# Optimization experiments

Measured on AMD Instinct MI355X. Metric: run time of the kernel, lower is better.

The kernel has to match this reference:

```python
import jax, jax.numpy as jnp
import numpy as np

E, T, IN, OUT = 8, 16384, 1024, 1024  # n_groups, total_tokens, in_features, out_features


def setup_inputs() -> dict:
    key = jax.random.key(0)
    kx, kw, ks = jax.random.split(key, 3)
    x = jax.random.normal(kx, (T, IN), dtype=jnp.float32)
    # kaiming_uniform-ish scale for weight [E, OUT, IN]
    weight = jax.random.normal(kw, (E, OUT, IN), dtype=jnp.float32) * (1.0 / np.sqrt(IN))
    # ragged segment lengths that sum exactly to T (random cut points)
    cuts = jnp.sort(jax.random.randint(ks, (E - 1,), 0, T + 1)).astype(jnp.int32)
    seg_lens = jnp.diff(
        jnp.concatenate([jnp.zeros((1,), jnp.int32), cuts, jnp.full((1,), T, jnp.int32)])
    )
    return {"x": x, "weight": weight, "seg_lens": seg_lens}


def reference(x, weight, seg_lens):
    # Grouped GEMM: row t of x is multiplied by weight[g(t)].T where g(t) is the
    # segment (expert) that token t falls into per seg_lens. trans_b=True.
    n_groups = weight.shape[0]
    bounds = jnp.cumsum(seg_lens)                                  # [E]
    seg_id = jnp.searchsorted(bounds, jnp.arange(x.shape[0]), side="right")  # [T]
    y = jnp.zeros((x.shape[0], weight.shape[1]), dtype=x.dtype)
    for e in range(n_groups):  # small fixed loop over groups
        y = y + jnp.where((seg_id == e)[:, None], x @ weight[e].T, 0)
    return y
```

## Files before the change

kernel.cpp:

```cpp
#include <hip/hip_runtime.h>

#define T_TOK  16384
#define IN_F   1024
#define OUT_F  1024
#define NE     8

typedef __bf16 bf16;
typedef bf16  bf16x4 __attribute__((ext_vector_type(4)));
typedef bf16  bf16x8 __attribute__((ext_vector_type(8)));
typedef float f32x4  __attribute__((ext_vector_type(4)));

#define BM 256
#define BN 256
#define BK 64
#define GTHREADS 512
#define NBLOCKS 256
#define KCH (IN_F / BK)
#define SP_BLOCKS 112

#define CVT_THREADS 256
#define NX_CHUNKS (T_TOK * IN_F / 4)
#define NW_CHUNKS (NE * OUT_F * IN_F / 4)
#define NCVT_CHUNKS (NX_CHUNKS + NW_CHUNKS)

__global__ __launch_bounds__(CVT_THREADS)
void cvt_and_zero(const float* __restrict__ x, const float* __restrict__ w,
                  bf16* __restrict__ xb, bf16* __restrict__ wb,
                  const int* __restrict__ seg_lens, float* __restrict__ out)
{
    int r64 = T_TOK;
    {
        int slots = 0, start = 0;
        #pragma unroll
        for (int e = 0; e < NE; ++e) {
            int len = seg_lens[e];
            int nt  = (len + BM - 1) >> 8;
            if (slots <= 64 && slots + nt > 64) {
                r64 = start + (64 - slots) * BM;
            }
            slots += nt;
            start += len;
        }
    }
    const int zero_chunks = (T_TOK - r64) * (OUT_F / 4);
    const int zbase       = r64 * (OUT_F / 4);
    const int tot         = NCVT_CHUNKS + zero_chunks;

    for (int i = blockIdx.x * CVT_THREADS + threadIdx.x; i < tot;
         i += gridDim.x * CVT_THREADS) {
        if (i < NCVT_CHUNKS) {
            const bool isx = (i < NX_CHUNKS);
            const int  j   = isx ? i : i - NX_CHUNKS;
            f32x4 v = isx ? ((const f32x4*)x)[j] : ((const f32x4*)w)[j];
            bf16x4 h;
            #pragma unroll
            for (int k = 0; k < 4; ++k) h[k] = (bf16)v[k];
            if (isx) ((bf16x4*)xb)[j] = h;
            else     ((bf16x4*)wb)[j] = h;
        } else {
            f32x4 z = {0.f, 0.f, 0.f, 0.f};
            ((f32x4*)out)[zbase + (i - NCVT_CHUNKS)] = z;
        }
    }
}

__device__ __forceinline__ void gld_lds16(const bf16* g, bf16* l) {
    __builtin_amdgcn_global_load_lds(
        (const __attribute__((address_space(1))) void*)g,
        (__attribute__((address_space(3))) void*)l,
        16, 0, 0);
}

__device__ __forceinline__ void resolve_slot(const int* sl, int slot,
                                             int& e_sel, int& row0, int& rows)
{
    e_sel = -1; row0 = 0; rows = 0;
    int start = 0, acct = 0;
    #pragma unroll
    for (int e = 0; e < NE; ++e) {
        int len = sl[e];
        int nt  = (len + BM - 1) >> 8;
        if (e_sel < 0 && slot >= acct && slot < acct + nt) {
            e_sel = e;
            row0  = start + (slot - acct) * BM;
            int rm = start + len - row0;
            rows = rm < BM ? rm : BM;
        }
        acct  += nt;
        start += len;
    }
}

__global__ __launch_bounds__(GTHREADS)
void grouped_gemm_main(const bf16* __restrict__ xb,
                       const bf16* __restrict__ wb,
                       const int*  __restrict__ seg_lens,
                       float* __restrict__ out)
{
    __shared__ __align__(16) bf16 As[2][BM * BK];
    __shared__ __align__(16) bf16 Bs[2][BN * BK];

    const int tile = blockIdx.x;
    const int slot = tile >> 2;
    const int col0 = (tile & 3) << 8;

    int sl[NE];
    #pragma unroll
    for (int e = 0; e < NE; ++e) sl[e] = seg_lens[e];

    int e_sel, row0, rows;
    resolve_slot(sl, slot, e_sel, row0, rows);
    if (e_sel < 0) return;

    const int tid  = threadIdx.x;
    const int lane = tid & 63;
    const int wave = tid >> 6;
    const int wr   = wave >> 2;
    const int wc   = wave & 3;
    const int quad = lane >> 4;
    const int l16  = lane & 15;
    const int rq   = lane >> 3;
    const int ke   = (lane & 7) * 8;
    const int q0   = wave * 4;

    const bf16* wbase = wb + ((size_t)e_sel * OUT_F + (size_t)col0) * IN_F;

    const bf16* ga[4];
    const bf16* gb[4];
    #pragma unroll
    for (int i = 0; i < 4; ++i) {
        int q  = wave * 4 + i;
        int ra = row0 + q * 8 + rq;
        if (ra > T_TOK - 1) ra = T_TOK - 1;
        ga[i] = xb + (size_t)ra * IN_F + ke;
        gb[i] = wbase + (size_t)(q * 8 + rq) * IN_F + ke;
    }

    f32x4 acc[8][4] = {};

    #pragma unroll
    for (int i = 0; i < 4; ++i) {
        gld_lds16(ga[i], &As[0][(q0 + i) * 512]);
        gld_lds16(gb[i], &Bs[0][(q0 + i) * 512]);
    }
    __syncthreads();

    int cur = 0;
    for (int ks = 0; ks < KCH; ++ks) {
        const int kn = (ks + 1) * BK;
        if (kn < IN_F) {
            #pragma unroll
            for (int i = 0; i < 4; ++i) {
                gld_lds16(ga[i] + kn, &As[cur ^ 1][(q0 + i) * 512]);
                gld_lds16(gb[i] + kn, &Bs[cur ^ 1][(q0 + i) * 512]);
            }
        }

        #pragma unroll
        for (int kk = 0; kk < 2; ++kk) {
            bf16x8 af[8], bfr[4];
            #pragma unroll
            for (int t = 0; t < 8; ++t)
                af[t] = *(const bf16x8*)(
                    &As[cur][(wr * 128 + t * 16 + l16) * BK + kk * 32 + quad * 8]);
            #pragma unroll
            for (int v = 0; v < 4; ++v)
                bfr[v] = *(const bf16x8*)(
                    &Bs[cur][(wc * 64 + v * 16 + l16) * BK + kk * 32 + quad * 8]);
            #pragma unroll
            for (int t = 0; t < 8; ++t)
                #pragma unroll
                for (int v = 0; v < 4; ++v)
                    acc[t][v] = __builtin_amdgcn_mfma_f32_16x16x32_bf16(
                        af[t], bfr[v], acc[t][v], 0, 0, 0);
        }

        __syncthreads();
        cur ^= 1;
    }

    #pragma unroll
    for (int t = 0; t < 8; ++t) {
        #pragma unroll
        for (int r = 0; r < 4; ++r) {
            int row = wr * 128 + t * 16 + quad * 4 + r;
            if (row < rows) {
                size_t ob = (size_t)(row0 + row) * OUT_F + col0 + wc * 64;
                #pragma unroll
                for (int v = 0; v < 4; ++v)
                    out[ob + v * 16 + l16] = acc[t][v][r];
            }
        }
    }
}

__global__ __launch_bounds__(GTHREADS)
void grouped_gemm_surplus(const bf16* __restrict__ xb,
                          const bf16* __restrict__ wb,
                          const int*  __restrict__ seg_lens,
                          float* __restrict__ out)
{
    __shared__ __align__(16) bf16 As[2][BM * BK];
    __shared__ __align__(16) bf16 Bs[2][BN * BK];

    const int tile   = NBLOCKS + (blockIdx.x >> 2);
    const int kslice = blockIdx.x & 3;

    int sl[NE];
    #pragma unroll
    for (int e = 0; e < NE; ++e) sl[e] = seg_lens[e];

    int n_slots = 0;
    #pragma unroll
    for (int e = 0; e < NE; ++e) n_slots += (sl[e] + BM - 1) >> 8;
    const int L = n_slots * (OUT_F / BN);
    if (tile >= L) return;

    const int slot = tile >> 2;
    const int col0 = (tile & 3) << 8;
    int e_sel, row0, rows;
    resolve_slot(sl, slot, e_sel, row0, rows);

    const int tid  = threadIdx.x;
    const int lane = tid & 63;
    const int wave = tid >> 6;
    const int wr   = wave >> 2;
    const int wc   = wave & 3;
    const int quad = lane >> 4;
    const int l16  = lane & 15;
    const int rq   = lane >> 3;
    const int ke   = (lane & 7) * 8;
    const int q0   = wave * 4;

    const bf16* wbase = wb + ((size_t)e_sel * OUT_F + (size_t)col0) * IN_F;

    const bf16* ga[4];
    const bf16* gb[4];
    #pragma unroll
    for (int i = 0; i < 4; ++i) {
        int q  = wave * 4 + i;
        int ra = row0 + q * 8 + rq;
        if (ra > T_TOK - 1) ra = T_TOK - 1;
        ga[i] = xb + (size_t)ra * IN_F + ke;
        gb[i] = wbase + (size_t)(q * 8 + rq) * IN_F + ke;
    }

    f32x4 acc[8][4] = {};

    const int kb0 = kslice * 4 * BK;

    #pragma unroll
    for (int i = 0; i < 4; ++i) {
        gld_lds16(ga[i] + kb0, &As[0][(q0 + i) * 512]);
        gld_lds16(gb[i] + kb0, &Bs[0][(q0 + i) * 512]);
    }
    __syncthreads();

    #pragma unroll
    for (int j = 0; j < 4; ++j) {
        const int cur = j & 1;
        if (j < 3) {
            const int kn = kb0 + (j + 1) * BK;
            #pragma unroll
            for (int i = 0; i < 4; ++i) {
                gld_lds16(ga[i] + kn, &As[cur ^ 1][(q0 + i) * 512]);
                gld_lds16(gb[i] + kn, &Bs[cur ^ 1][(q0 + i) * 512]);
            }
        }

        #pragma unroll
        for (int kk = 0; kk < 2; ++kk) {
            bf16x8 af[8], bfr[4];
            #pragma unroll
            for (int t = 0; t < 8; ++t)
                af[t] = *(const bf16x8*)(
                    &As[cur][(wr * 128 + t * 16 + l16) * BK + kk * 32 + quad * 8]);
            #pragma unroll
            for (int v = 0; v < 4; ++v)
                bfr[v] = *(const bf16x8*)(
                    &Bs[cur][(wc * 64 + v * 16 + l16) * BK + kk * 32 + quad * 8]);
            #pragma unroll
            for (int t = 0; t < 8; ++t)
                #pragma unroll
                for (int v = 0; v < 4; ++v)
                    acc[t][v] = __builtin_amdgcn_mfma_f32_16x16x32_bf16(
                        af[t], bfr[v], acc[t][v], 0, 0, 0);
        }

        __syncthreads();
    }

    #pragma unroll
    for (int t = 0; t < 8; ++t) {
        #pragma unroll
        for (int r = 0; r < 4; ++r) {
            int row = wr * 128 + t * 16 + quad * 4 + r;
            if (row < rows) {
                size_t ob = (size_t)(row0 + row) * OUT_F + col0 + wc * 64;
                #pragma unroll
                for (int v = 0; v < 4; ++v)
                    unsafeAtomicAdd(&out[ob + v * 16 + l16], acc[t][v][r]);
            }
        }
    }
}

#define FBM 128
#define FBK 32
#define FTHREADS 256
#define FROW_SLOTS 136

__global__ __launch_bounds__(FTHREADS)
void grouped_gemm_f32io_bf16(const float* __restrict__ x,
                             const float* __restrict__ wgt,
                             const int*  __restrict__ seg_lens,
                             float* __restrict__ out)
{
    __shared__ __align__(16) bf16 Asf[FBM * FBK];
    __shared__ __align__(16) bf16 Bsf[FBM * FBK];

    const int m    = blockIdx.y;
    const int col0 = blockIdx.x * FBM;

    int e_sel = -1, row0 = 0, rows = 0;
    {
        int start = 0, acct = 0;
        #pragma unroll
        for (int e = 0; e < NE; ++e) {
            int len = seg_lens[e];
            int nt  = (len + FBM - 1) >> 7;
            if (e_sel < 0 && m >= acct && m < acct + nt) {
                e_sel = e;
                row0  = start + (m - acct) * FBM;
                int rem = start + len - row0;
                rows = rem < FBM ? rem : FBM;
            }
            acct  += nt;
            start += len;
        }
    }
    if (e_sel < 0) return;

    const int tid  = threadIdx.x;
    const int lane = tid & 63;
    const int wave = tid >> 6;
    const int wm   = (wave >> 1) * 64;
    const int wn   = (wave & 1) * 64;
    const int quad = lane >> 4;
    const int l16  = lane & 15;

    const float* wbase = wgt + ((size_t)e_sel * OUT_F + (size_t)col0) * IN_F;

    f32x4 acc[4][4] = {};

    for (int k0 = 0; k0 < IN_F; k0 += FBK) {
        f32x4 a_st[4], b_st[4];
        #pragma unroll
        for (int t = 0; t < 4; ++t) {
            int c  = t * FTHREADS + tid;
            int rg = row0 + (c >> 3);
            if (rg > T_TOK - 1) rg = T_TOK - 1;
            a_st[t] = *(const f32x4*)(x + (size_t)rg * IN_F + k0 + (c & 7) * 4);
            b_st[t] = *(const f32x4*)(wbase + (size_t)(c >> 3) * IN_F + k0 + (c & 7) * 4);
        }

        __syncthreads();

        #pragma unroll
        for (int t = 0; t < 4; ++t) {
            int c = t * FTHREADS + tid;
            bf16x4 ha, hb;
            #pragma unroll
            for (int j = 0; j < 4; ++j) { ha[j] = (bf16)a_st[t][j]; hb[j] = (bf16)b_st[t][j]; }
            *(bf16x4*)(&Asf[(c >> 3) * FBK + (c & 7) * 4]) = ha;
            *(bf16x4*)(&Bsf[(c >> 3) * FBK + (c & 7) * 4]) = hb;
        }
        __syncthreads();

        bf16x8 af[4], bfr[4];
        #pragma unroll
        for (int t = 0; t < 4; ++t)
            af[t] = *(const bf16x8*)(&Asf[(wm + t * 16 + l16) * FBK + quad * 8]);
        #pragma unroll
        for (int v = 0; v < 4; ++v)
            bfr[v] = *(const bf16x8*)(&Bsf[(wn + v * 16 + l16) * FBK + quad * 8]);

        #pragma unroll
        for (int t = 0; t < 4; ++t)
            #pragma unroll
            for (int v = 0; v < 4; ++v)
                acc[t][v] = __builtin_amdgcn_mfma_f32_16x16x32_bf16(
                    af[t], bfr[v], acc[t][v], 0, 0, 0);
    }

    #pragma unroll
    for (int t = 0; t < 4; ++t) {
        #pragma unroll
        for (int r = 0; r < 4; ++r) {
            int row = wm + t * 16 + quad * 4 + r;
            if (row < rows) {
                size_t ob = (size_t)(row0 + row) * OUT_F + col0;
                #pragma unroll
                for (int v = 0; v < 4; ++v)
                    out[ob + wn + v * 16 + l16] = acc[t][v][r];
            }
        }
    }
}

extern "C" void kernel_launch(void* const* d_in, const int* in_sizes, int n_in,
                              void* d_out, int out_size, void* d_ws, size_t ws_size,
                              hipStream_t stream) {
    const float* x   = (const float*)d_in[0];
    const float* wgt = (const float*)d_in[1];
    const int*   seg = (const int*)d_in[2];
    float* out = (float*)d_out;

    const size_t xbytes = (size_t)T_TOK * IN_F * sizeof(bf16);
    const size_t wbytes = (size_t)NE * OUT_F * IN_F * sizeof(bf16);

    if (ws_size >= xbytes + wbytes) {
        bf16* xb = (bf16*)d_ws;
        bf16* wb = (bf16*)((char*)d_ws + xbytes);
        cvt_and_zero<<<dim3(2048, 1, 1), dim3(CVT_THREADS, 1, 1), 0, stream>>>(
            x, wgt, xb, wb, seg, out);
        grouped_gemm_main<<<dim3(NBLOCKS, 1, 1), dim3(GTHREADS, 1, 1), 0, stream>>>(
            xb, wb, seg, out);
        grouped_gemm_surplus<<<dim3(SP_BLOCKS, 1, 1), dim3(GTHREADS, 1, 1), 0, stream>>>(
            xb, wb, seg, out);
    } else {
        grouped_gemm_f32io_bf16<<<dim3(OUT_F / FBM, FROW_SLOTS, 1),
                                  dim3(FTHREADS, 1, 1), 0, stream>>>(x, wgt, seg, out);
    }
}
```

Baseline: 215.0 us.

## Swizzle LDS tiles, use explicit vmcnt waits in GEMM pipeline, widen conversion vectors

The main GEMM kernel now XOR-swizzles the k-chunk position of each row when loading into LDS and applies the matching swizzle on fragment reads, to remove LDS bank conflicts. The k-loop is restructured so the next tile's loads are issued first, then a partial s_waitcnt vmcnt(8) and raw barriers with sched_barrier fences gate the compute, letting the prefetch stay in flight during MFMA work. The conversion kernel processes 8 elements per thread instead of 4. The hand-written waitcnt and barriers depend on exact load counts and ordering, so any mismatch could give incorrect results.

```diff
diff --git a/kernel.cpp b/kernel.cpp
--- a/kernel.cpp
+++ b/kernel.cpp
@@ -19,9 +19,9 @@
 #define SP_BLOCKS 112
 
 #define CVT_THREADS 256
-#define NX_CHUNKS (T_TOK * IN_F / 4)
-#define NW_CHUNKS (NE * OUT_F * IN_F / 4)
-#define NCVT_CHUNKS (NX_CHUNKS + NW_CHUNKS)
+#define NX8 (T_TOK * IN_F / 8)
+#define NW8 (NE * OUT_F * IN_F / 8)
+#define NCVT8 (NX8 + NW8)
 
 __global__ __launch_bounds__(CVT_THREADS)
 void cvt_and_zero(const float* __restrict__ x, const float* __restrict__ w,
@@ -42,24 +42,27 @@
             start += len;
         }
     }
-    const int zero_chunks = (T_TOK - r64) * (OUT_F / 4);
-    const int zbase       = r64 * (OUT_F / 4);
-    const int tot         = NCVT_CHUNKS + zero_chunks;
+    const int zero8 = (T_TOK - r64) * (OUT_F / 8);
+    const int zb8   = r64 * (OUT_F / 8);
+    const int tot   = NCVT8 + zero8;
 
     for (int i = blockIdx.x * CVT_THREADS + threadIdx.x; i < tot;
          i += gridDim.x * CVT_THREADS) {
-        if (i < NCVT_CHUNKS) {
-            const bool isx = (i < NX_CHUNKS);
-            const int  j   = isx ? i : i - NX_CHUNKS;
-            f32x4 v = isx ? ((const f32x4*)x)[j] : ((const f32x4*)w)[j];
-            bf16x4 h;
-            #pragma unroll
-            for (int k = 0; k < 4; ++k) h[k] = (bf16)v[k];
-            if (isx) ((bf16x4*)xb)[j] = h;
-            else     ((bf16x4*)wb)[j] = h;
+        if (i < NCVT8) {
+            const bool isx = (i < NX8);
+            const int  j   = isx ? i : i - NX8;
+            f32x4 v0 = isx ? ((const f32x4*)x)[2*j]   : ((const f32x4*)w)[2*j];
+            f32x4 v1 = isx ? ((const f32x4*)x)[2*j+1] : ((const f32x4*)w)[2*j+1];
+            bf16x8 h;
+            #pragma unroll
+            for (int k = 0; k < 4; ++k) { h[k] = (bf16)v0[k]; h[4+k] = (bf16)v1[k]; }
+            if (isx) ((bf16x8*)xb)[j] = h;
+            else     ((bf16x8*)wb)[j] = h;
         } else {
             f32x4 z = {0.f, 0.f, 0.f, 0.f};
-            ((f32x4*)out)[zbase + (i - NCVT_CHUNKS)] = z;
+            const int j = zb8 + (i - NCVT8);
+            ((f32x4*)out)[2*j]   = z;
+            ((f32x4*)out)[2*j+1] = z;
         }
     }
 }
@@ -91,6 +94,31 @@
     }
 }
 
+__device__ __forceinline__ void mfma_step(const bf16* __restrict__ Ab,
+                                          const bf16* __restrict__ Bb,
+                                          f32x4 (&acc)[8][4],
+                                          int wr, int wc, int l16, int quad,
+                                          int swz8)
+{
+    #pragma unroll
+    for (int kk = 0; kk < 2; ++kk) {
+        const int ce = (kk * 32 + quad * 8) ^ swz8;
+        bf16x8 af[8], bfr[4];
+        #pragma unroll
+        for (int t = 0; t < 8; ++t)
+            af[t] = *(const bf16x8*)(Ab + (wr * 128 + t * 16 + l16) * BK + ce);
+        #pragma unroll
+        for (int v = 0; v < 4; ++v)
+            bfr[v] = *(const bf16x8*)(Bb + (wc * 64 + v * 16 + l16) * BK + ce);
+        #pragma unroll
+        for (int t = 0; t < 8; ++t)
+            #pragma unroll
+            for (int v = 0; v < 4; ++v)
+                acc[t][v] = __builtin_amdgcn_mfma_f32_16x16x32_bf16(
+                    af[t], bfr[v], acc[t][v], 0, 0, 0);
+    }
+}
+
 __global__ __launch_bounds__(GTHREADS)
 void grouped_gemm_main(const bf16* __restrict__ xb,
                        const bf16* __restrict__ wb,
@@ -120,8 +148,10 @@
     const int quad = lane >> 4;
     const int l16  = lane & 15;
     const int rq   = lane >> 3;
-    const int ke   = (lane & 7) * 8;
     const int q0   = wave * 4;
+    const int swz8 = (l16 & 7) * 8;
+
+    const int ke_s = (((lane & 7) ^ rq) * 8);
 
     const bf16* wbase = wb + ((size_t)e_sel * OUT_F + (size_t)col0) * IN_F;
 
@@ -132,8 +162,8 @@
         int q  = wave * 4 + i;
         int ra = row0 + q * 8 + rq;
         if (ra > T_TOK - 1) ra = T_TOK - 1;
-        ga[i] = xb + (size_t)ra * IN_F + ke;
-        gb[i] = wbase + (size_t)(q * 8 + rq) * IN_F + ke;
+        ga[i] = xb + (size_t)ra * IN_F + ke_s;
+        gb[i] = wbase + (size_t)(q * 8 + rq) * IN_F + ke_s;
     }
 
     f32x4 acc[8][4] = {};
@@ -143,41 +173,27 @@
         gld_lds16(ga[i], &As[0][(q0 + i) * 512]);
         gld_lds16(gb[i], &Bs[0][(q0 + i) * 512]);
     }
-    __syncthreads();
-
-    int cur = 0;
-    for (int ks = 0; ks < KCH; ++ks) {
-        const int kn = (ks + 1) * BK;
-        if (kn < IN_F) {
-            #pragma unroll
-            for (int i = 0; i < 4; ++i) {
-                gld_lds16(ga[i] + kn, &As[cur ^ 1][(q0 + i) * 512]);
-                gld_lds16(gb[i] + kn, &Bs[cur ^ 1][(q0 + i) * 512]);
-            }
-        }
-
-        #pragma unroll
-        for (int kk = 0; kk < 2; ++kk) {
-            bf16x8 af[8], bfr[4];
-            #pragma unroll
-            for (int t = 0; t < 8; ++t)
-                af[t] = *(const bf16x8*)(
-                    &As[cur][(wr * 128 + t * 16 + l16) * BK + kk * 32 + quad * 8]);
-            #pragma unroll
-            for (int v = 0; v < 4; ++v)
-                bfr[v] = *(const bf16x8*)(
-                    &Bs[cur][(wc * 64 + v * 16 + l16) * BK + kk * 32 + quad * 8]);
-            #pragma unroll
-            for (int t = 0; t < 8; ++t)
-                #pragma unroll
-                for (int v = 0; v < 4; ++v)
-                    acc[t][v] = __builtin_amdgcn_mfma_f32_16x16x32_bf16(
-                        af[t], bfr[v], acc[t][v], 0, 0, 0);
-        }
-
-        __syncthreads();
-        cur ^= 1;
-    }
+
+    for (int n = 0; n < KCH - 1; ++n) {
+        const int kn  = (n + 1) * BK;
+        const int nxt = (n + 1) & 1;
+        #pragma unroll
+        for (int i = 0; i < 4; ++i) {
+            gld_lds16(ga[i] + kn, &As[nxt][(q0 + i) * 512]);
+            gld_lds16(gb[i] + kn, &Bs[nxt][(q0 + i) * 512]);
+        }
+        asm volatile("s_waitcnt vmcnt(8)" ::: "memory");
+        __builtin_amdgcn_s_barrier();
+        __builtin_amdgcn_sched_barrier(0);
+        mfma_step(&As[n & 1][0], &Bs[n & 1][0], acc, wr, wc, l16, quad, swz8);
+        __builtin_amdgcn_sched_barrier(0);
+        __builtin_amdgcn_s_barrier();
+    }
+    asm volatile("s_waitcnt vmcnt(0)" ::: "memory");
+    __builtin_amdgcn_s_barrier();
+    __builtin_amdgcn_sched_barrier(0);
+    mfma_step(&As[(KCH - 1) & 1][0], &Bs[(KCH - 1) & 1][0], acc,
+              wr, wc, l16, quad, swz8);
 
     #pragma unroll
     for (int t = 0; t < 8; ++t) {
```

New measurement: 205.5 us. 4.4% less time.
